# Performance work log

Hardware: AMD Instinct MI355X
Metric: run time of the kernel (lower is better)

Reference implementation:

```python
import jax, jax.numpy as jnp
import numpy as np

UNITS = 128
Q_DIM = 256
V_DIM = 256
BATCH = 128
SEQ = 4096


def setup_inputs() -> dict:
    key = jax.random.key(0)
    ks = jax.random.split(key, 8)
    query = jax.random.normal(ks[0], (BATCH, Q_DIM), dtype=jnp.float32)
    values = jax.random.normal(ks[1], (BATCH, SEQ, V_DIM), dtype=jnp.float32)
    # Dense params (glorot-ish scale)
    W1 = jax.random.normal(ks[2], (Q_DIM, UNITS), dtype=jnp.float32) * (1.0 / np.sqrt(Q_DIM))
    b1 = jnp.zeros((UNITS,), dtype=jnp.float32)
    W2 = jax.random.normal(ks[3], (V_DIM, UNITS), dtype=jnp.float32) * (1.0 / np.sqrt(V_DIM))
    b2 = jnp.zeros((UNITS,), dtype=jnp.float32)
    Wv = jax.random.normal(ks[4], (UNITS, 1), dtype=jnp.float32) * (1.0 / np.sqrt(UNITS))
    bv = jnp.zeros((1,), dtype=jnp.float32)
    return {"query": query, "values": values, "W1": W1, "b1": b1,
            "W2": W2, "b2": b2, "Wv": Wv, "bv": bv}


def reference(query, values, W1, b1, W2, b2, Wv, bv):
    # q_proj: [B, 1, U]; v_proj: [B, S, U]
    q_proj = (query @ W1 + b1)[:, None, :]
    v_proj = jnp.einsum('bsd,du->bsu', values, W2) + b2
    # score: [B, S, 1]
    score = jnp.tanh(q_proj + v_proj) @ Wv + bv
    attention_weights = jax.nn.softmax(score, axis=1)  # softmax over seq_len
    context = jnp.sum(attention_weights * values, axis=1)  # [B, V_DIM]
    return (context, attention_weights)
```

## Files before the change

### kernel.cpp

```cpp
#include <hip/hip_runtime.h>

#define B_ 128
#define S_ 4096
#define D_ 256
#define U_ 128
#define CR_ 64
#define NCH_ 32
#define HALF_ROWS 2048
#define PITCH 264

typedef _Float16 half8 __attribute__((ext_vector_type(8)));
typedef _Float16 half4_t __attribute__((ext_vector_type(4)));
typedef float f32x4 __attribute__((ext_vector_type(4)));


__global__ void qp_kernel(const float* __restrict__ query,
                          const float* __restrict__ W1,
                          const float* __restrict__ b1,
                          const float* __restrict__ b2,
                          float* __restrict__ qp) {
  const int idx = blockIdx.x * 256 + threadIdx.x;
  const int b = idx >> 7;
  const int u = idx & 127;
  float acc = b1[u] + b2[u];
  const float* q = query + b * D_;
  #pragma unroll 8
  for (int d = 0; d < D_; ++d) acc += q[d] * W1[d * U_ + u];
  qp[idx] = acc;
}

__global__ void w2t_kernel(const float* __restrict__ W2,
                           _Float16* __restrict__ w2t) {
  const int idx = blockIdx.x * 256 + threadIdx.x;
  const int u = idx >> 8;
  const int d = idx & 255;
  w2t[idx] = (_Float16)W2[d * U_ + u];
}


__global__ __launch_bounds__(512)
void main_kernel(const float* __restrict__ values,
                 const float* __restrict__ qp,
                 const _Float16* __restrict__ w2t,
                 const float* __restrict__ Wv,
                 const float* __restrict__ bv,
                 float* __restrict__ scores,
                 float* __restrict__ part) {
  __shared__ _Float16 Alds[CR_][PITCH];
  __shared__ _Float16 Blds[U_][PITCH];
  __shared__ float sb[2][CR_];
  __shared__ float p_sh[CR_];
  __shared__ float qp_sh[U_];
  __shared__ float wv_sh[U_];
  __shared__ float ctxpart[16][D_];
  __shared__ float bc[4];

  const int t = threadIdx.x;
  const int b = blockIdx.x >> 1;
  const int half = blockIdx.x & 1;
  const int lane = t & 63;
  const int wave = t >> 6;

  const half8* __restrict__ wsrc = (const half8*)w2t;
  #pragma unroll
  for (int i = 0; i < 8; ++i) {
    const int idx = t + i * 512;
    const int u = idx >> 5;
    const int d8 = idx & 31;
    *(half8*)&Blds[u][d8 * 8] = wsrc[idx];
  }
  if (t < U_) { qp_sh[t] = qp[b * U_ + t]; wv_sh[t] = Wv[t]; }
  if (t == 0) bc[3] = bv[0];

  const f32x4* __restrict__ vbase =
      (const f32x4*)(values + ((size_t)b * S_ + half * HALF_ROWS) * D_);

  {
    f32x4 v[8];
    #pragma unroll
    for (int i = 0; i < 8; ++i) v[i] = vbase[t + i * 512];
    #pragma unroll
    for (int i = 0; i < 8; ++i) {
      const int idx = t + i * 512;
      const int row = idx >> 6;
      const int d4 = idx & 63;
      half4_t h;
      h[0] = (_Float16)v[i][0]; h[1] = (_Float16)v[i][1];
      h[2] = (_Float16)v[i][2]; h[3] = (_Float16)v[i][3];
      *(half4_t*)&Alds[row][d4 * 4] = h;
    }
  }
  __syncthreads();

  const int wr = (wave >> 1) * 16;
  const int wcg = wave & 1;
  const int wc = wcg * 64;
  const int lm = lane & 15;
  const int lq = lane >> 4;
  const int lk = lq * 8;

  float qpv[4], wvv[4];
  #pragma unroll
  for (int nt = 0; nt < 4; ++nt) {
    const int u = wc + nt * 16 + lm;
    qpv[nt] = qp_sh[u];
    wvv[nt] = wv_sh[u];
  }

  float M = -INFINITY, L = 0.0f;
  float cacc[8];
  #pragma unroll
  for (int j = 0; j < 8; ++j) cacc[j] = 0.0f;
  const int rg = t >> 5;
  const int v8 = (t & 31) * 8;

  for (int c = 0; c < NCH_; ++c) {
    f32x4 pf[8];
    if (c + 1 < NCH_) {
      const f32x4* __restrict__ src = vbase + (size_t)(c + 1) * (CR_ * 64);
      #pragma unroll
      for (int i = 0; i < 8; ++i) pf[i] = src[t + i * 512];
    }

    f32x4 acc[4];
    const f32x4 zero = {0.0f, 0.0f, 0.0f, 0.0f};
    #pragma unroll
    for (int nt = 0; nt < 4; ++nt) acc[nt] = zero;
    #pragma unroll
    for (int k = 0; k < 8; ++k) {
      const int kb = k * 32 + lk;
      half8 af = *(const half8*)&Alds[wr + lm][kb];
      #pragma unroll
      for (int nt = 0; nt < 4; ++nt) {
        half8 bf = *(const half8*)&Blds[wc + nt * 16 + lm][kb];
        acc[nt] = __builtin_amdgcn_mfma_f32_16x16x32_f16(af, bf, acc[nt], 0, 0, 0);
      }
    }

    float rs[4] = {0.0f, 0.0f, 0.0f, 0.0f};
    #pragma unroll
    for (int nt = 0; nt < 4; ++nt) {
      #pragma unroll
      for (int r = 0; r < 4; ++r) {
        const float x = acc[nt][r] + qpv[nt];
        const float e = __expf(2.0f * x);
        rs[r] += (1.0f - 2.0f / (e + 1.0f)) * wvv[nt];
      }
    }
    #pragma unroll
    for (int r = 0; r < 4; ++r) {
      float v = rs[r];
      v += __shfl_xor(v, 1);
      v += __shfl_xor(v, 2);
      v += __shfl_xor(v, 4);
      v += __shfl_xor(v, 8);
      if (lm == 0) sb[wcg][wr + lq * 4 + r] = v;
    }
    __syncthreads();

    if (t < CR_) {
      const float sc = sb[0][t] + sb[1][t] + bc[3];
      scores[(size_t)b * S_ + half * HALF_ROWS + c * CR_ + t] = sc;
      float mv = sc;
      mv = fmaxf(mv, __shfl_xor(mv, 1));
      mv = fmaxf(mv, __shfl_xor(mv, 2));
      mv = fmaxf(mv, __shfl_xor(mv, 4));
      mv = fmaxf(mv, __shfl_xor(mv, 8));
      mv = fmaxf(mv, __shfl_xor(mv, 16));
      mv = fmaxf(mv, __shfl_xor(mv, 32));
      const float m_new = fmaxf(M, mv);
      const float p = __expf(sc - m_new);
      p_sh[t] = p;
      float lv = p;
      lv += __shfl_xor(lv, 1);
      lv += __shfl_xor(lv, 2);
      lv += __shfl_xor(lv, 4);
      lv += __shfl_xor(lv, 8);
      lv += __shfl_xor(lv, 16);
      lv += __shfl_xor(lv, 32);
      if (t == 0) { bc[0] = m_new; bc[1] = lv; bc[2] = __expf(M - m_new); }
    }
    __syncthreads();

    const float alpha = bc[2];
    const float l_c = bc[1];
    M = bc[0];
    L = L * alpha + l_c;

    #pragma unroll
    for (int j = 0; j < 8; ++j) cacc[j] *= alpha;
    #pragma unroll
    for (int r = 0; r < 4; ++r) {
      const int row = rg * 4 + r;
      const float pr = p_sh[row];
      half8 hv = *(const half8*)&Alds[row][v8];
      #pragma unroll
      for (int j = 0; j < 8; ++j) cacc[j] += pr * (float)hv[j];
    }
    __syncthreads();

    if (c + 1 < NCH_) {
      #pragma unroll
      for (int i = 0; i < 8; ++i) {
        const int idx = t + i * 512;
        const int row = idx >> 6;
        const int d4 = idx & 63;
        half4_t h;
        h[0] = (_Float16)pf[i][0]; h[1] = (_Float16)pf[i][1];
        h[2] = (_Float16)pf[i][2]; h[3] = (_Float16)pf[i][3];
        *(half4_t*)&Alds[row][d4 * 4] = h;
      }
    }
    __syncthreads();
  }

  #pragma unroll
  for (int j = 0; j < 8; ++j) ctxpart[rg][v8 + j] = cacc[j];
  __syncthreads();
  if (t < D_) {
    float s = 0.0f;
    #pragma unroll
    for (int g = 0; g < 16; ++g) s += ctxpart[g][t];
    const size_t base = (size_t)blockIdx.x * 258;
    part[base + 2 + t] = s;
    if (t == 0) { part[base] = M; part[base + 1] = L; }
  }
}


__global__ void combine_kernel(const float* __restrict__ part,
                               float* __restrict__ ml,
                               float* __restrict__ out_ctx) {
  const int b = blockIdx.x;
  const int t = threadIdx.x;
  const size_t b0 = (size_t)(b * 2) * 258;
  const size_t b1 = b0 + 258;
  const float m0 = part[b0], l0 = part[b0 + 1];
  const float m1 = part[b1], l1 = part[b1 + 1];
  const float Mf = fmaxf(m0, m1);
  const float s0 = __expf(m0 - Mf);
  const float s1 = __expf(m1 - Mf);
  const float Lf = l0 * s0 + l1 * s1;
  out_ctx[b * D_ + t] = (part[b0 + 2 + t] * s0 + part[b1 + 2 + t] * s1) / Lf;
  if (t == 0) { ml[b * 2] = Mf; ml[b * 2 + 1] = Lf; }
}


__global__ void weights_kernel(const float* __restrict__ scores,
                               const float* __restrict__ ml,
                               float* __restrict__ out_w) {
  const int idx = blockIdx.x * 256 + threadIdx.x;
  const int b = idx >> 12;
  const float M = ml[b * 2];
  const float L = ml[b * 2 + 1];
  out_w[idx] = __expf(scores[idx] - M) / L;
}


extern "C" void kernel_launch(void* const* d_in, const int* in_sizes, int n_in,
                              void* d_out, int out_size, void* d_ws, size_t ws_size,
                              hipStream_t stream) {
  const float* query  = (const float*)d_in[0];
  const float* values = (const float*)d_in[1];
  const float* W1     = (const float*)d_in[2];
  const float* b1     = (const float*)d_in[3];
  const float* W2     = (const float*)d_in[4];
  const float* b2     = (const float*)d_in[5];
  const float* Wv     = (const float*)d_in[6];
  const float* bv     = (const float*)d_in[7];

  float* out_ctx = (float*)d_out;
  float* out_w   = out_ctx + B_ * D_;

  char* ws = (char*)d_ws;
  float*     qp     = (float*)ws;
  _Float16*  w2t    = (_Float16*)(ws + 65536);
  float*     scores = (float*)(ws + 131072);
  float*     part   = (float*)(ws + 131072 + 2097152);
  float*     ml     = (float*)(ws + 131072 + 2097152 + 264192);

  qp_kernel<<<dim3(64), dim3(256), 0, stream>>>(query, W1, b1, b2, qp);
  w2t_kernel<<<dim3(128), dim3(256), 0, stream>>>(W2, w2t);
  main_kernel<<<dim3(B_ * 2), dim3(512), 0, stream>>>(values, qp, w2t, Wv, bv,
                                                      scores, part);
  combine_kernel<<<dim3(B_), dim3(256), 0, stream>>>(part, ml, out_ctx);
  weights_kernel<<<dim3(B_ * S_ / 256), dim3(256), 0, stream>>>(scores, ml, out_w);
}
```

Before: 732.8 us.

## Split sequence into four slices, keep W2 in registers, double-buffer LDS

Each batch row is now split into four sequence slices instead of two, giving 512 blocks so more CUs are busy. The W2 tile moves from LDS into per-wave registers with the MFMA operands swapped, which frees LDS for a double-buffered values tile and removes one barrier per chunk. The softmax statistics are computed redundantly in every wave and shared through shuffles rather than a serial single-wave pass. The combine kernel merges four partial results, and register pressure rises under the new launch bound.

```diff
diff --git a/kernel.cpp b/kernel.cpp
--- a/kernel.cpp
+++ b/kernel.cpp
@@ -5,8 +5,9 @@
 #define D_ 256
 #define U_ 128
 #define CR_ 64
-#define NCH_ 32
-#define HALF_ROWS 2048
+#define NSL_ 4
+#define SLR_ 1024
+#define NCH_ 16
 #define PITCH 264
 
 typedef _Float16 half8 __attribute__((ext_vector_type(8)));
@@ -38,7 +39,7 @@
 }
 
 
-__global__ __launch_bounds__(512)
+__global__ __launch_bounds__(512, 4)
 void main_kernel(const float* __restrict__ values,
                  const float* __restrict__ qp,
                  const _Float16* __restrict__ w2t,
@@ -46,34 +47,21 @@
                  const float* __restrict__ bv,
                  float* __restrict__ scores,
                  float* __restrict__ part) {
-  __shared__ _Float16 Alds[CR_][PITCH];
-  __shared__ _Float16 Blds[U_][PITCH];
-  __shared__ float sb[2][CR_];
-  __shared__ float p_sh[CR_];
-  __shared__ float qp_sh[U_];
-  __shared__ float wv_sh[U_];
-  __shared__ float ctxpart[16][D_];
-  __shared__ float bc[4];
+  __shared__ __align__(16) char smem[2 * CR_ * PITCH * 2];
+  _Float16 (*Alds)[CR_][PITCH] = (_Float16 (*)[CR_][PITCH])smem;
+  __shared__ float sb[8][CR_];
 
   const int t = threadIdx.x;
-  const int b = blockIdx.x >> 1;
-  const int half = blockIdx.x & 1;
+  const int b = blockIdx.x >> 2;
+  const int sl = blockIdx.x & 3;
   const int lane = t & 63;
   const int wave = t >> 6;
-
-  const half8* __restrict__ wsrc = (const half8*)w2t;
-  #pragma unroll
-  for (int i = 0; i < 8; ++i) {
-    const int idx = t + i * 512;
-    const int u = idx >> 5;
-    const int d8 = idx & 31;
-    *(half8*)&Blds[u][d8 * 8] = wsrc[idx];
-  }
-  if (t < U_) { qp_sh[t] = qp[b * U_ + t]; wv_sh[t] = Wv[t]; }
-  if (t == 0) bc[3] = bv[0];
+  const int lm = lane & 15;
+  const int lq = lane >> 4;
+  const int lk = lq * 8;
 
   const f32x4* __restrict__ vbase =
-      (const f32x4*)(values + ((size_t)b * S_ + half * HALF_ROWS) * D_);
+      (const f32x4*)(values + ((size_t)b * S_ + (size_t)sl * SLR_) * D_);
 
   {
     f32x4 v[8];
@@ -87,25 +75,23 @@
       half4_t h;
       h[0] = (_Float16)v[i][0]; h[1] = (_Float16)v[i][1];
       h[2] = (_Float16)v[i][2]; h[3] = (_Float16)v[i][3];
-      *(half4_t*)&Alds[row][d4 * 4] = h;
-    }
-  }
+      *(half4_t*)&Alds[0][row][d4 * 4] = h;
+    }
+  }
+
+  half8 breg[8];
+  {
+    const half8* __restrict__ wp =
+        (const half8*)(w2t + (size_t)(wave * 16 + lm) * D_);
+    #pragma unroll
+    for (int kk = 0; kk < 8; ++kk) breg[kk] = wp[kk * 4 + lq];
+  }
+  const int ub = wave * 16 + lq * 4;
+  const f32x4 qv  = *(const f32x4*)(qp + (size_t)b * U_ + ub);
+  const f32x4 wv4 = *(const f32x4*)(Wv + ub);
+  const float bvv = bv[0];
+
   __syncthreads();
-
-  const int wr = (wave >> 1) * 16;
-  const int wcg = wave & 1;
-  const int wc = wcg * 64;
-  const int lm = lane & 15;
-  const int lq = lane >> 4;
-  const int lk = lq * 8;
-
-  float qpv[4], wvv[4];
-  #pragma unroll
-  for (int nt = 0; nt < 4; ++nt) {
-    const int u = wc + nt * 16 + lm;
-    qpv[nt] = qp_sh[u];
-    wvv[nt] = wv_sh[u];
-  }
 
   float M = -INFINITY, L = 0.0f;
   float cacc[8];
@@ -115,6 +101,8 @@
   const int v8 = (t & 31) * 8;
 
   for (int c = 0; c < NCH_; ++c) {
+    const int cur = c & 1;
+
     f32x4 pf[8];
     if (c + 1 < NCH_) {
       const f32x4* __restrict__ src = vbase + (size_t)(c + 1) * (CR_ * 64);
@@ -125,79 +113,66 @@
     f32x4 acc[4];
     const f32x4 zero = {0.0f, 0.0f, 0.0f, 0.0f};
     #pragma unroll
-    for (int nt = 0; nt < 4; ++nt) acc[nt] = zero;
-    #pragma unroll
-    for (int k = 0; k < 8; ++k) {
-      const int kb = k * 32 + lk;
-      half8 af = *(const half8*)&Alds[wr + lm][kb];
-      #pragma unroll
-      for (int nt = 0; nt < 4; ++nt) {
-        half8 bf = *(const half8*)&Blds[wc + nt * 16 + lm][kb];
-        acc[nt] = __builtin_amdgcn_mfma_f32_16x16x32_f16(af, bf, acc[nt], 0, 0, 0);
+    for (int rt = 0; rt < 4; ++rt) acc[rt] = zero;
+    #pragma unroll
+    for (int kk = 0; kk < 8; ++kk) {
+      #pragma unroll
+      for (int rt = 0; rt < 4; ++rt) {
+        half8 af = *(const half8*)&Alds[cur][rt * 16 + lm][kk * 32 + lk];
+        acc[rt] = __builtin_amdgcn_mfma_f32_16x16x32_f16(breg[kk], af, acc[rt], 0, 0, 0);
       }
     }
 
-    float rs[4] = {0.0f, 0.0f, 0.0f, 0.0f};
-    #pragma unroll
-    for (int nt = 0; nt < 4; ++nt) {
+    #pragma unroll
+    for (int rt = 0; rt < 4; ++rt) {
+      float rs = 0.0f;
       #pragma unroll
       for (int r = 0; r < 4; ++r) {
-        const float x = acc[nt][r] + qpv[nt];
+        const float x = acc[rt][r] + qv[r];
         const float e = __expf(2.0f * x);
-        rs[r] += (1.0f - 2.0f / (e + 1.0f)) * wvv[nt];
+        rs += (1.0f - 2.0f / (e + 1.0f)) * wv4[r];
       }
-    }
-    #pragma unroll
-    for (int r = 0; r < 4; ++r) {
-      float v = rs[r];
-      v += __shfl_xor(v, 1);
-      v += __shfl_xor(v, 2);
-      v += __shfl_xor(v, 4);
-      v += __shfl_xor(v, 8);
-      if (lm == 0) sb[wcg][wr + lq * 4 + r] = v;
+      rs += __shfl_xor(rs, 16);
+      rs += __shfl_xor(rs, 32);
+      if (lq == 0) sb[wave][rt * 16 + lm] = rs;
     }
     __syncthreads();
 
-    if (t < CR_) {
-      const float sc = sb[0][t] + sb[1][t] + bc[3];
-      scores[(size_t)b * S_ + half * HALF_ROWS + c * CR_ + t] = sc;
-      float mv = sc;
-      mv = fmaxf(mv, __shfl_xor(mv, 1));
-      mv = fmaxf(mv, __shfl_xor(mv, 2));
-      mv = fmaxf(mv, __shfl_xor(mv, 4));
-      mv = fmaxf(mv, __shfl_xor(mv, 8));
-      mv = fmaxf(mv, __shfl_xor(mv, 16));
-      mv = fmaxf(mv, __shfl_xor(mv, 32));
-      const float m_new = fmaxf(M, mv);
-      const float p = __expf(sc - m_new);
-      p_sh[t] = p;
-      float lv = p;
-      lv += __shfl_xor(lv, 1);
-      lv += __shfl_xor(lv, 2);
-      lv += __shfl_xor(lv, 4);
-      lv += __shfl_xor(lv, 8);
-      lv += __shfl_xor(lv, 16);
-      lv += __shfl_xor(lv, 32);
-      if (t == 0) { bc[0] = m_new; bc[1] = lv; bc[2] = __expf(M - m_new); }
-    }
-    __syncthreads();
-
-    const float alpha = bc[2];
-    const float l_c = bc[1];
-    M = bc[0];
-    L = L * alpha + l_c;
+    float sc = bvv;
+    #pragma unroll
+    for (int w = 0; w < 8; ++w) sc += sb[w][lane];
+    if (wave == 0)
+      scores[(size_t)b * S_ + (size_t)sl * SLR_ + c * CR_ + lane] = sc;
+    float mv = sc;
+    mv = fmaxf(mv, __shfl_xor(mv, 1));
+    mv = fmaxf(mv, __shfl_xor(mv, 2));
+    mv = fmaxf(mv, __shfl_xor(mv, 4));
+    mv = fmaxf(mv, __shfl_xor(mv, 8));
+    mv = fmaxf(mv, __shfl_xor(mv, 16));
+    mv = fmaxf(mv, __shfl_xor(mv, 32));
+    const float m_new = fmaxf(M, mv);
+    const float p = __expf(sc - m_new);
+    float lv = p;
+    lv += __shfl_xor(lv, 1);
+    lv += __shfl_xor(lv, 2);
+    lv += __shfl_xor(lv, 4);
+    lv += __shfl_xor(lv, 8);
+    lv += __shfl_xor(lv, 16);
+    lv += __shfl_xor(lv, 32);
+    const float alpha = __expf(M - m_new);
+    M = m_new;
+    L = L * alpha + lv;
 
     #pragma unroll
     for (int j = 0; j < 8; ++j) cacc[j] *= alpha;
     #pragma unroll
     for (int r = 0; r < 4; ++r) {
       const int row = rg * 4 + r;
-      const float pr = p_sh[row];
-      half8 hv = *(const half8*)&Alds[row][v8];
+      const float pr = __shfl(p, row);
+      half8 hv = *(const half8*)&Alds[cur][row][v8];
       #pragma unroll
       for (int j = 0; j < 8; ++j) cacc[j] += pr * (float)hv[j];
     }
-    __syncthreads();
 
     if (c + 1 < NCH_) {
       #pragma unroll
@@ -208,12 +183,13 @@
         half4_t h;
         h[0] = (_Float16)pf[i][0]; h[1] = (_Float16)pf[i][1];
         h[2] = (_Float16)pf[i][2]; h[3] = (_Float16)pf[i][3];
-        *(half4_t*)&Alds[row][d4 * 4] = h;
+        *(half4_t*)&Alds[cur ^ 1][row][d4 * 4] = h;
       }
     }
     __syncthreads();
   }
 
+  float (*ctxpart)[D_] = (float (*)[D_])smem;
   #pragma unroll
   for (int j = 0; j < 8; ++j) ctxpart[rg][v8 + j] = cacc[j];
   __syncthreads();
@@ -233,15 +209,19 @@
                                float* __restrict__ out_ctx) {
   const int b = blockIdx.x;
   const int t = threadIdx.x;
-  const size_t b0 = (size_t)(b * 2) * 258;
-  const size_t b1 = b0 + 258;
-  const float m0 = part[b0], l0 = part[b0 + 1];
-  const float m1 = part[b1], l1 = part[b1 + 1];
-  const float Mf = fmaxf(m0, m1);
+  const size_t p0 = (size_t)b * 4 * 258;
+  const float m0 = part[p0],           l0 = part[p0 + 1];
+  const float m1 = part[p0 + 258],     l1 = part[p0 + 258 + 1];
+  const float m2 = part[p0 + 516],     l2 = part[p0 + 516 + 1];
+  const float m3 = part[p0 + 774],     l3 = part[p0 + 774 + 1];
+  const float Mf = fmaxf(fmaxf(m0, m1), fmaxf(m2, m3));
   const float s0 = __expf(m0 - Mf);
   const float s1 = __expf(m1 - Mf);
-  const float Lf = l0 * s0 + l1 * s1;
-  out_ctx[b * D_ + t] = (part[b0 + 2 + t] * s0 + part[b1 + 2 + t] * s1) / Lf;
+  const float s2 = __expf(m2 - Mf);
+  const float s3 = __expf(m3 - Mf);
+  const float Lf = l0 * s0 + l1 * s1 + l2 * s2 + l3 * s3;
+  out_ctx[b * D_ + t] = (part[p0 + 2 + t] * s0 + part[p0 + 258 + 2 + t] * s1 +
+                         part[p0 + 516 + 2 + t] * s2 + part[p0 + 774 + 2 + t] * s3) / Lf;
   if (t == 0) { ml[b * 2] = Mf; ml[b * 2 + 1] = Lf; }
 }
 
@@ -277,12 +257,12 @@
   _Float16*  w2t    = (_Float16*)(ws + 65536);
   float*     scores = (float*)(ws + 131072);
   float*     part   = (float*)(ws + 131072 + 2097152);
-  float*     ml     = (float*)(ws + 131072 + 2097152 + 264192);
+  float*     ml     = (float*)(ws + 131072 + 2097152 + 528384);
 
   qp_kernel<<<dim3(64), dim3(256), 0, stream>>>(query, W1, b1, b2, qp);
   w2t_kernel<<<dim3(128), dim3(256), 0, stream>>>(W2, w2t);
-  main_kernel<<<dim3(B_ * 2), dim3(512), 0, stream>>>(values, qp, w2t, Wv, bv,
-                                                      scores, part);
+  main_kernel<<<dim3(B_ * NSL_), dim3(512), 0, stream>>>(values, qp, w2t, Wv, bv,
+                                                         scores, part);
   combine_kernel<<<dim3(B_), dim3(256), 0, stream>>>(part, ml, out_ctx);
   weights_kernel<<<dim3(B_ * S_ / 256), dim3(256), 0, stream>>>(scores, ml, out_w);
 }
```

Result: no change. 723.5 us (-1.3%).
